# Kernel optimization log

Measured on AMD Instinct MI355X. Metric: run time of the kernel, lower is better.

The kernel has to match this reference:

```python
import jax, jax.numpy as jnp
import numpy as np

BL = 512  # block length (matches init bl)


def _conv1x1(w, b, x):
    # w: (out, in), b: (out,), x: (batch, in, L) -> (batch, out, L)
    return jnp.einsum('oi,bil->bol', w, x) + b[None, :, None]


def _window_mask(bl):
    # Faithful to torch loop: window_mask[:, :, i:i+bl] = 1 for i in range(bl)
    # -> all ones except the last column.
    wm = np.zeros((1, bl, bl + 2 * (bl // 2)), np.float32)
    for i in range(bl):
        wm[:, :, i:i + bl] = 1.0
    return jnp.asarray(wm)


def setup_inputs() -> dict:
    key = jax.random.key(0)
    ks = jax.random.split(key, 5)
    B, C, L = 1, 2048, 16384
    Cq = C // 2  # r1 = r2 = r3 = 2
    s_in = 1.0 / float(np.sqrt(C))
    s_mid = 1.0 / float(np.sqrt(Cq))
    return {
        'x1': jax.random.normal(ks[0], (B, C, L), jnp.float32),
        'x2': jnp.zeros((B, C, L), jnp.float32),
        'mask': jnp.ones((B, 1, L), jnp.float32),
        'wq': jax.random.normal(ks[1], (Cq, C), jnp.float32) * s_in,
        'bq': jnp.zeros((Cq,), jnp.float32),
        'wk': jax.random.normal(ks[2], (Cq, C), jnp.float32) * s_in,
        'bk': jnp.zeros((Cq,), jnp.float32),
        'wv': jax.random.normal(ks[3], (Cq, C), jnp.float32) * s_in,
        'bv': jnp.zeros((Cq,), jnp.float32),
        'wo': jax.random.normal(ks[4], (C, Cq), jnp.float32) * s_mid,
        'bo': jnp.zeros((C,), jnp.float32),
    }


def reference(x1, x2, mask, wq, bq, wk, bk, wv, bv, wo, bo):
    B, C, L = x1.shape  # B == 1 (asserted by sliding path)
    bl = BL
    nb = L // bl  # L % bl == 0 by construction
    half = bl // 2

    q = _conv1x1(wq, bq, x1)  # (1, c, L)
    k = _conv1x1(wk, bk, x1)
    v = _conv1x1(wv, bv, x1)  # encoder stage: value from x1 (x2 unused)
    c = q.shape[1]

    # query blocks: (nb, c, bl)
    qb = q.reshape(B, c, nb, bl).transpose(0, 2, 1, 3).reshape(nb, c, bl)

    # pad k/v/padding_mask with bl//2 zeros on both sides, then take overlapping
    # windows of width 2*bl per block.
    kp = jnp.pad(k, ((0, 0), (0, 0), (half, half)))[0]            # (c, L+bl)
    vp = jnp.pad(v, ((0, 0), (0, 0), (half, half)))[0]
    pm = jnp.pad(mask[:, 0:1, :], ((0, 0), (0, 0), (half, half)))[0]  # (1, L+bl)
    cols = np.arange(nb)[:, None] * bl + np.arange(2 * bl)[None, :]   # (nb, 2bl)
    kb = kp[:, cols].transpose(1, 0, 2)   # (nb, c, 2bl)
    vb = vp[:, cols].transpose(1, 0, 2)   # (nb, c, 2bl)
    pmb = pm[:, cols].transpose(1, 0, 2)  # (nb, 1, 2bl)

    final_mask = _window_mask(bl) * pmb   # (nb, bl, 2bl)

    # scalar dot attention with log-mask (as in AttentionHelper.scalar_dot_att)
    energy = jnp.einsum('ncl,ncm->nlm', qb, kb) / jnp.float32(np.sqrt(c))
    attn = jax.nn.softmax(energy + jnp.log(final_mask + 1e-9), axis=-1)
    attn = attn * final_mask
    out = jnp.einsum('ncm,nlm->ncl', vb, attn)  # (nb, c, bl)

    out = _conv1x1(wo, bo, jax.nn.relu(out))    # (nb, C, bl)
    out = out.reshape(B, nb, C, bl).transpose(0, 2, 1, 3).reshape(B, C, nb * bl)
    out = out[:, :, :L]
    return out * mask[:, 0:1, :]
```

## Files before the change

### kernel.cpp

```cpp
#include <hip/hip_runtime.h>
#include <hip/hip_bf16.h>

typedef __attribute__((ext_vector_type(4))) float f32x4;
typedef __attribute__((ext_vector_type(8))) __bf16 bf16x8;

struct ushort4_t { unsigned short x, y, z, w; };

#define DEVINL static __device__ __forceinline__

DEVINL unsigned short f2bf(float f) {
  union { float f; unsigned u; } x; x.f = f;
  return (unsigned short)((x.u + 0x7FFFu + ((x.u >> 16) & 1u)) >> 16);
}

DEVINL void gload16(const void* g, void* l) {
  __builtin_amdgcn_global_load_lds((const __attribute__((address_space(1))) void*)g,
                                   (__attribute__((address_space(3))) void*)l,
                                   16, 0, 0);
}

#define SBAR()   asm volatile("s_barrier" ::: "memory")
#define LGKM0()  asm volatile("s_waitcnt lgkmcnt(0)" ::: "memory")
#define LGKM8()  asm volatile("s_waitcnt lgkmcnt(8)" ::: "memory")
#define VM(n)    asm volatile("s_waitcnt vmcnt(" #n ")" ::: "memory")

__global__ __launch_bounds__(256) void transpose_x_k(const float* __restrict__ x,
                                                     unsigned short* __restrict__ xT) {
  __shared__ float tile[32][33];
  const int bx = blockIdx.x;
  const int by = blockIdx.y;
  const int tx = threadIdx.x;
  const int ty = threadIdx.y;
#pragma unroll
  for (int i = 0; i < 4; ++i) {
    int c = by * 32 + ty + i * 8;
    tile[ty + i * 8][tx] = x[(long)c * 16384 + bx * 32 + tx];
  }
  __syncthreads();
  const int t = ty * 32 + tx;
  const int lrow = t >> 3;
  const int cq = (t & 7) << 2;
  ushort4_t o;
  o.x = f2bf(tile[cq + 0][lrow]);
  o.y = f2bf(tile[cq + 1][lrow]);
  o.z = f2bf(tile[cq + 2][lrow]);
  o.w = f2bf(tile[cq + 3][lrow]);
  *reinterpret_cast<ushort4_t*>(xT + (long)(bx * 32 + lrow) * 2048 + by * 32 + cq) = o;
}

__global__ __launch_bounds__(256) void conv_w_k(const float* __restrict__ wq,
                                                const float* __restrict__ wk,
                                                const float* __restrict__ wv,
                                                const float* __restrict__ wo,
                                                unsigned short* __restrict__ Wqk,
                                                unsigned short* __restrict__ Wv,
                                                unsigned short* __restrict__ Wo) {
  long i = ((long)blockIdx.x * 256 + threadIdx.x) * 4;
  const float* src;
  unsigned short* dst;
  if (i < 4194304) {
    src = (i < 2097152) ? (wq + i) : (wk + i - 2097152);
    dst = Wqk + i;
  } else if (i < 6291456) {
    src = wv + (i - 4194304);
    dst = Wv + (i - 4194304);
  } else {
    src = wo + (i - 6291456);
    dst = Wo + (i - 6291456);
  }
  float4 v = *reinterpret_cast<const float4*>(src);
  ushort4_t o{f2bf(v.x), f2bf(v.y), f2bf(v.z), f2bf(v.w)};
  *reinterpret_cast<ushort4_t*>(dst) = o;
}

enum { EPI_QK = 0, EPI_V = 1, EPI_S = 2, EPI_PV = 3, EPI_OUT = 4 };

struct GArgs {
  const unsigned short* A;
  const unsigned short* Bt;
  void* C;
  const float* bias;
  const float* bias2;
  const float* mask;
  const unsigned short* guard;
  int aBatch, cBatch;
  int btRow0, btRow0Step, btRowLim;
  int btK0, btK0Step, btKLim;
};

template <int EPI, int GUARDED, int LDA, int LDB, int LDC, int KK>
__global__ __launch_bounds__(512, 2) void gemm8_k(GArgs g) {
  constexpr int NK = KK >> 6;
  constexpr int NT = NK >> 1;
  __shared__ char lds[131072];

  const int t = threadIdx.x;
  const int l = t & 63;
  const int w = t >> 6;

  const int gx = gridDim.x, gxy = gx * gridDim.y;
  const int nwg = gxy * gridDim.z;
  int lin = blockIdx.z * gxy + blockIdx.y * gx + blockIdx.x;
  lin = (lin & 7) * (nwg >> 3) + (lin >> 3);
  const int z = lin / gxy;
  const int rres = lin - z * gxy;
  const int Mbase = (rres / gx) << 8;
  const int Nbase = (rres - (rres / gx) * gx) << 8;

  const int wr = w >> 2;
  const int wc = w & 3;
  const int fr = l & 15;
  const int fg = l >> 4;

  const unsigned short* Ab = g.A + (long)z * g.aBatch + (long)Mbase * LDA;
  const int bRowBase = g.btRow0 + z * g.btRow0Step + Nbase;
  const int bK0 = g.btK0 + z * g.btK0Step;

  const int rr = t >> 3;
  const int cb8s = t & 7;
  const int cbL = cb8s ^ (rr & 7);
  const int bRowT = (rr & 31) + ((rr >> 5) << 6);
  const char* aStageG = (const char*)(Ab + (long)rr * LDA) + (cbL << 4);
  const char* bStageG = (const char*)(g.Bt + (long)(bRowBase + bRowT) * LDB + bK0) + (cbL << 4);
  char* aStageL = lds + rr * 128 + (cb8s << 4);
  char* bStageL = lds + 65536 + bRowT * 128 + (cb8s << 4);

  auto stage = [&](int bufSel, int unit, int kt) {
    const int k0b = (kt & (NK - 1)) << 7;
    const bool isA = (unit == 0) || (unit == 3);
#pragma unroll
    for (int gph = 0; gph < 2; ++gph) {
      const int rowAdd = (isA ? (unit == 0 ? 0 : 64) : (unit == 1 ? 0 : 32)) + (gph << 7);
      if (isA) {
        gload16(aStageG + (long)rowAdd * (LDA * 2) + k0b,
                aStageL + bufSel * 32768 + rowAdd * 128);
      } else if (!GUARDED) {
        gload16(bStageG + (long)rowAdd * (LDB * 2) + k0b,
                bStageL + bufSel * 32768 + rowAdd * 128);
      } else {
        const int row = rowAdd + bRowT;
        const int gk = ((kt & (NK - 1)) << 6) + (cbL << 3);
        const int grow = bRowBase + row;
        const int gkk = bK0 + gk;
        const char* gp =
            ((unsigned)grow < (unsigned)g.btRowLim && (unsigned)gkk < (unsigned)g.btKLim)
                ? (const char*)(g.Bt + (long)grow * LDB + gkk)
                : (const char*)g.guard + (l << 4);
        gload16(gp, bStageL + bufSel * 32768 + rowAdd * 128);
      }
    }
  };

  const int arow = (wr << 7) + fr;
  const int brow = (wc << 6) + fr;
  const int sA = arow & 7, sB = brow & 7;
  const char* aRd0 = lds + arow * 128 + ((fg ^ sA) << 4);
  const char* aRd1 = lds + arow * 128 + (((4 | fg) ^ sA) << 4);
  const char* bRd0 = lds + 65536 + brow * 128 + ((fg ^ sB) << 4);
  const char* bRd1 = lds + 65536 + brow * 128 + (((4 | fg) ^ sB) << 4);

  f32x4 acc[8][4];
#pragma unroll
  for (int i = 0; i < 8; ++i)
#pragma unroll
    for (int j = 0; j < 4; ++j) acc[i][j] = f32x4{0.f, 0.f, 0.f, 0.f};

  stage(0, 0, 0); stage(0, 1, 0); stage(0, 2, 0); stage(0, 3, 0);
  stage(1, 0, 1); stage(1, 1, 1); stage(1, 2, 1);
  VM(6);
  SBAR();

  bf16x8 fa[4][2], fb[4][2];

#define RA(slot, i8, B) \
  { fa[slot][0] = *(const bf16x8*)(aRd0 + ((B)*32768 + (i8)*2048)); \
    fa[slot][1] = *(const bf16x8*)(aRd1 + ((B)*32768 + (i8)*2048)); }
#define RB(j, B) \
  { fb[j][0] = *(const bf16x8*)(bRd0 + ((B)*32768 + (j)*2048)); \
    fb[j][1] = *(const bf16x8*)(bRd1 + ((B)*32768 + (j)*2048)); }

#define MFMA_Q(QI, QJ)                                                        \
  __builtin_amdgcn_s_setprio(1);                                              \
  _Pragma("unroll") for (int kk = 0; kk < 2; ++kk)                            \
  _Pragma("unroll") for (int i = 0; i < 4; ++i)                               \
  _Pragma("unroll") for (int j = 0; j < 2; ++j)                               \
    acc[(QI)*4 + i][(QJ)*2 + j] = __builtin_amdgcn_mfma_f32_16x16x32_bf16(    \
        fa[i][kk], fb[(QJ)*2 + j][kk], acc[(QI)*4 + i][(QJ)*2 + j], 0, 0, 0); \
  __builtin_amdgcn_s_setprio(0);

#pragma unroll 1
  for (int it = 0; it < NT; ++it) {
    const int kt1 = 2 * it + 1;
    const int ktn0 = 2 * it + 2;
    const int ktn1 = 2 * it + 3;
    RA(0, 0, 0) RA(1, 1, 0) RA(2, 2, 0) RA(3, 3, 0)
    RB(0, 0) RB(1, 0)
    stage(1, 3, kt1);
    LGKM8();
    SBAR(); LGKM0();
    MFMA_Q(0, 0);
    SBAR();
    RB(2, 0) RB(3, 0)
    stage(0, 0, ktn0);
    SBAR(); LGKM0();
    MFMA_Q(0, 1);
    SBAR();
    RA(0, 4, 0) RA(1, 5, 0) RA(2, 6, 0) RA(3, 7, 0)
    stage(0, 1, ktn0);
    SBAR(); LGKM0();
    MFMA_Q(1, 0);
    SBAR();
    stage(0, 2, ktn0);
    SBAR(); LGKM0();
    MFMA_Q(1, 1);
    VM(6);
    SBAR();
    RA(0, 0, 1) RA(1, 1, 1) RA(2, 2, 1) RA(3, 3, 1)
    RB(0, 1) RB(1, 1)
    stage(0, 3, ktn0);
    LGKM8();
    SBAR(); LGKM0();
    MFMA_Q(0, 0);
    SBAR();
    RB(2, 1) RB(3, 1)
    stage(1, 0, ktn1);
    SBAR(); LGKM0();
    MFMA_Q(0, 1);
    SBAR();
    RA(0, 4, 1) RA(1, 5, 1) RA(2, 6, 1) RA(3, 7, 1)
    stage(1, 1, ktn1);
    SBAR(); LGKM0();
    MFMA_Q(1, 0);
    SBAR();
    stage(1, 2, ktn1);
    SBAR(); LGKM0();
    MFMA_Q(1, 1);
    VM(6);
    SBAR();
  }
  VM(0); LGKM0(); SBAR();

#pragma unroll
  for (int ii = 0; ii < 8; ++ii)
#pragma unroll
    for (int j = 0; j < 4; ++j)
#pragma unroll
      for (int r = 0; r < 4; ++r) {
        const int row = Mbase + (wr << 7) + ii * 16 + fg * 4 + r;
        const int col = Nbase + (wc << 6) + j * 16 + fr;
        float val = acc[ii][j][r];
        const long off = (long)z * g.cBatch + (long)row * LDC + col;
        if (EPI == EPI_QK) {
          val = (col < 1024) ? (val + g.bias[col]) * 0.03125f
                             : (val + g.bias2[col - 1024]);
          ((unsigned short*)g.C)[off] = f2bf(val);
        } else if (EPI == EPI_V) {
          val += g.bias[row];
          ((unsigned short*)g.C)[off] = f2bf(val);
        } else if (EPI == EPI_S) {
          ((float*)g.C)[off] = val;
        } else if (EPI == EPI_PV) {
          val = fmaxf(val, 0.f);
          ((unsigned short*)g.C)[off] = f2bf(val);
        } else {
          val = (val + g.bias[row]) * g.mask[col];
          ((float*)g.C)[off] = val;
        }
      }
#undef MFMA_Q
#undef RA
#undef RB
}

__global__ __launch_bounds__(256) void softmax_k(const float* __restrict__ S,
                                                 const float* __restrict__ mask,
                                                 unsigned short* __restrict__ P) {
  const int row = blockIdx.x;
  const int n = row >> 9;
  const float* s = S + (long)row * 1024;
  unsigned short* p = P + (long)row * 1024;
  const int t = threadIdx.x;

  const float4 sv = *reinterpret_cast<const float4*>(s + t * 4);
  const int pos0 = (n << 9) + t * 4 - 256;
  float4 mv = {0.f, 0.f, 0.f, 0.f};
  if ((unsigned)pos0 < 16384u) mv = *reinterpret_cast<const float4*>(mask + pos0);
  float fm[4] = {mv.x, mv.y, mv.z, mv.w};
  if (t == 255) fm[3] = 0.f;
  const float sc[4] = {sv.x, sv.y, sv.z, sv.w};

  float logit[4];
  float lmax = -3.0e38f;
#pragma unroll
  for (int k = 0; k < 4; ++k) {
    logit[k] = sc[k] + logf(fm[k] + 1e-9f);
    lmax = fmaxf(lmax, logit[k]);
  }
#pragma unroll
  for (int o = 32; o; o >>= 1) lmax = fmaxf(lmax, __shfl_xor(lmax, o, 64));
  __shared__ float red[8];
  const int wv_ = t >> 6, ln = t & 63;
  if (ln == 0) red[wv_] = lmax;
  __syncthreads();
  const float gmax = fmaxf(fmaxf(red[0], red[1]), fmaxf(red[2], red[3]));

  float e[4], lsum = 0.f;
#pragma unroll
  for (int k = 0; k < 4; ++k) { e[k] = expf(logit[k] - gmax); lsum += e[k]; }
#pragma unroll
  for (int o = 32; o; o >>= 1) lsum += __shfl_xor(lsum, o, 64);
  if (ln == 0) red[4 + wv_] = lsum;
  __syncthreads();
  const float inv = 1.f / ((red[4] + red[5]) + (red[6] + red[7]));
  ushort4_t o4;
  o4.x = f2bf(e[0] * inv * fm[0]);
  o4.y = f2bf(e[1] * inv * fm[1]);
  o4.z = f2bf(e[2] * inv * fm[2]);
  o4.w = f2bf(e[3] * inv * fm[3]);
  *reinterpret_cast<ushort4_t*>(p + t * 4) = o4;
}

extern "C" void kernel_launch(void* const* d_in, const int* in_sizes, int n_in,
                              void* d_out, int out_size, void* d_ws, size_t ws_size,
                              hipStream_t stream) {
  const float* x1 = (const float*)d_in[0];
  const float* mask = (const float*)d_in[2];
  const float* wq = (const float*)d_in[3];
  const float* bq = (const float*)d_in[4];
  const float* wk = (const float*)d_in[5];
  const float* bk = (const float*)d_in[6];
  const float* wv = (const float*)d_in[7];
  const float* bv = (const float*)d_in[8];
  const float* wo = (const float*)d_in[9];
  const float* bo = (const float*)d_in[10];

  char* ws = (char*)d_ws;
  unsigned short* xT   = (unsigned short*)(ws);
  unsigned short* attT = xT;
  unsigned short* Wqk  = (unsigned short*)(ws + 67108864);
  unsigned short* Wv   = (unsigned short*)(ws + 75497472);
  unsigned short* Wo   = (unsigned short*)(ws + 79691776);
  unsigned short* qkT  = (unsigned short*)(ws + 83886080);
  unsigned short* vbuf = (unsigned short*)(ws + 150994944);
  float*          Sbuf = (float*)(ws + 184549376);
  unsigned short* P    = (unsigned short*)(ws + 251658240);
  unsigned short* guard= (unsigned short*)(ws + 285212672);

  hipMemsetAsync(guard, 0, 4096, stream);

  transpose_x_k<<<dim3(512, 64), dim3(32, 8), 0, stream>>>(x1, xT);
  conv_w_k<<<dim3(8192), dim3(256), 0, stream>>>(wq, wk, wv, wo, Wqk, Wv, Wo);

  const int BIG = 0x40000000;
  {
    GArgs a{};
    a.A = xT; a.Bt = Wqk; a.C = qkT;
    a.bias = bq; a.bias2 = bk; a.guard = guard;
    a.aBatch = 0; a.cBatch = 0;
    a.btRow0 = 0; a.btRow0Step = 0; a.btRowLim = BIG;
    a.btK0 = 0; a.btK0Step = 0; a.btKLim = BIG;
    gemm8_k<EPI_QK, 0, 2048, 2048, 2048, 2048><<<dim3(8, 64, 1), 512, 0, stream>>>(a);
  }
  {
    GArgs a{};
    a.A = Wv; a.Bt = xT; a.C = vbuf;
    a.bias = bv; a.guard = guard;
    a.aBatch = 0; a.cBatch = 0;
    a.btRow0 = 0; a.btRow0Step = 0; a.btRowLim = BIG;
    a.btK0 = 0; a.btK0Step = 0; a.btKLim = BIG;
    gemm8_k<EPI_V, 0, 2048, 2048, 16384, 2048><<<dim3(64, 4, 1), 512, 0, stream>>>(a);
  }
  {
    GArgs a{};
    a.A = qkT; a.Bt = qkT; a.C = Sbuf;
    a.guard = guard;
    a.aBatch = 512 * 2048; a.cBatch = 512 * 1024;
    a.btRow0 = -256; a.btRow0Step = 512; a.btRowLim = 16384;
    a.btK0 = 1024; a.btK0Step = 0; a.btKLim = BIG;
    gemm8_k<EPI_S, 1, 2048, 2048, 1024, 1024><<<dim3(4, 2, 32), 512, 0, stream>>>(a);
  }
  softmax_k<<<dim3(16384), dim3(256), 0, stream>>>(Sbuf, mask, P);
  {
    GArgs a{};
    a.A = P; a.Bt = vbuf; a.C = attT;
    a.guard = guard;
    a.aBatch = 512 * 1024; a.cBatch = 512 * 1024;
    a.btRow0 = 0; a.btRow0Step = 0; a.btRowLim = BIG;
    a.btK0 = -256; a.btK0Step = 512; a.btKLim = 16384;
    gemm8_k<EPI_PV, 1, 1024, 16384, 1024, 1024><<<dim3(4, 2, 32), 512, 0, stream>>>(a);
  }
  {
    GArgs a{};
    a.A = Wo; a.Bt = attT; a.C = d_out;
    a.bias = bo; a.mask = mask; a.guard = guard;
    a.aBatch = 0; a.cBatch = 0;
    a.btRow0 = 0; a.btRow0Step = 0; a.btRowLim = BIG;
    a.btK0 = 0; a.btK0Step = 0; a.btKLim = BIG;
    gemm8_k<EPI_OUT, 0, 1024, 1024, 16384, 1024><<<dim3(64, 8, 1), 512, 0, stream>>>(a);
  }
  (void)in_sizes; (void)n_in; (void)out_size; (void)ws_size;
}
```

Before: 459.0 us.

## Simplify GEMM main loop to per-k-tile double buffering with fewer barriers

Replaces the hand-interleaved two-tile loop, which spread global-to-LDS stage loads between MFMA quarters with a barrier around each, with a simpler per-k-tile loop. The new loop reads all fragments from the current buffer, runs the MFMAs under sched_barrier and lgkmcnt waits, waits for all global loads, takes one barrier, then issues the next tile's loads into the freed buffer. This cuts barrier count and scheduling complexity but serialises global loads against compute more (VM(0) each iteration), and the stage calls at the end may read past KK unless stage guards the tile index.

```diff
diff --git a/kernel.cpp b/kernel.cpp
--- a/kernel.cpp
+++ b/kernel.cpp
@@ -20,9 +20,9 @@
 }
 
 #define SBAR()   asm volatile("s_barrier" ::: "memory")
-#define LGKM0()  asm volatile("s_waitcnt lgkmcnt(0)" ::: "memory")
-#define LGKM8()  asm volatile("s_waitcnt lgkmcnt(8)" ::: "memory")
+#define LGKM(n)  asm volatile("s_waitcnt lgkmcnt(" #n ")" ::: "memory")
 #define VM(n)    asm volatile("s_waitcnt vmcnt(" #n ")" ::: "memory")
+#define SCHED0() __builtin_amdgcn_sched_barrier(0)
 
 __global__ __launch_bounds__(256) void transpose_x_k(const float* __restrict__ x,
                                                      unsigned short* __restrict__ xT) {
@@ -91,7 +91,6 @@
 template <int EPI, int GUARDED, int LDA, int LDB, int LDC, int KK>
 __global__ __launch_bounds__(512, 2) void gemm8_k(GArgs g) {
   constexpr int NK = KK >> 6;
-  constexpr int NT = NK >> 1;
   __shared__ char lds[131072];
 
   const int t = threadIdx.x;
@@ -165,11 +164,6 @@
 #pragma unroll
     for (int j = 0; j < 4; ++j) acc[i][j] = f32x4{0.f, 0.f, 0.f, 0.f};
 
-  stage(0, 0, 0); stage(0, 1, 0); stage(0, 2, 0); stage(0, 3, 0);
-  stage(1, 0, 1); stage(1, 1, 1); stage(1, 2, 1);
-  VM(6);
-  SBAR();
-
   bf16x8 fa[4][2], fb[4][2];
 
 #define RA(slot, i8, B) \
@@ -188,57 +182,32 @@
         fa[i][kk], fb[(QJ)*2 + j][kk], acc[(QI)*4 + i][(QJ)*2 + j], 0, 0, 0); \
   __builtin_amdgcn_s_setprio(0);
 
+  stage(0, 0, 0); stage(0, 1, 0); stage(0, 2, 0); stage(0, 3, 0);
+  stage(1, 0, 1); stage(1, 1, 1); stage(1, 2, 1); stage(1, 3, 1);
+  VM(8);
+  SBAR();
+
 #pragma unroll 1
-  for (int it = 0; it < NT; ++it) {
-    const int kt1 = 2 * it + 1;
-    const int ktn0 = 2 * it + 2;
-    const int ktn1 = 2 * it + 3;
-    RA(0, 0, 0) RA(1, 1, 0) RA(2, 2, 0) RA(3, 3, 0)
-    RB(0, 0) RB(1, 0)
-    stage(1, 3, kt1);
-    LGKM8();
-    SBAR(); LGKM0();
+  for (int kt = 0; kt < NK; ++kt) {
+    const int cur = kt & 1;
+    RA(0, 0, cur) RA(1, 1, cur) RA(2, 2, cur) RA(3, 3, cur)
+    RB(0, cur) RB(1, cur)
+    SCHED0();
+    RB(2, cur) RB(3, cur)
+    LGKM(4); SCHED0();
     MFMA_Q(0, 0);
+    LGKM(0); SCHED0();
+    MFMA_Q(0, 1);
+    RA(0, 4, cur) RA(1, 5, cur) RA(2, 6, cur) RA(3, 7, cur)
+    LGKM(0); SCHED0();
+    MFMA_Q(1, 0);
+    MFMA_Q(1, 1);
+    VM(0);
     SBAR();
-    RB(2, 0) RB(3, 0)
-    stage(0, 0, ktn0);
-    SBAR(); LGKM0();
-    MFMA_Q(0, 1);
-    SBAR();
-    RA(0, 4, 0) RA(1, 5, 0) RA(2, 6, 0) RA(3, 7, 0)
-    stage(0, 1, ktn0);
-    SBAR(); LGKM0();
-    MFMA_Q(1, 0);
-    SBAR();
-    stage(0, 2, ktn0);
-    SBAR(); LGKM0();
-    MFMA_Q(1, 1);
-    VM(6);
-    SBAR();
-    RA(0, 0, 1) RA(1, 1, 1) RA(2, 2, 1) RA(3, 3, 1)
-    RB(0, 1) RB(1, 1)
-    stage(0, 3, ktn0);
-    LGKM8();
-    SBAR(); LGKM0();
-    MFMA_Q(0, 0);
-    SBAR();
-    RB(2, 1) RB(3, 1)
-    stage(1, 0, ktn1);
-    SBAR(); LGKM0();
-    MFMA_Q(0, 1);
-    SBAR();
-    RA(0, 4, 1) RA(1, 5, 1) RA(2, 6, 1) RA(3, 7, 1)
-    stage(1, 1, ktn1);
-    SBAR(); LGKM0();
-    MFMA_Q(1, 0);
-    SBAR();
-    stage(1, 2, ktn1);
-    SBAR(); LGKM0();
-    MFMA_Q(1, 1);
-    VM(6);
-    SBAR();
-  }
-  VM(0); LGKM0(); SBAR();
+    stage(cur, 0, kt + 2); stage(cur, 1, kt + 2);
+    stage(cur, 2, kt + 2); stage(cur, 3, kt + 2);
+  }
+  VM(0); LGKM(0); SBAR();
 
 #pragma unroll
   for (int ii = 0; ii < 8; ++ii)
```

Measured after the change: 467.1 us. About the same (+1.8%).
